# Kernel tuning notes

Hardware: AMD Instinct MI355X
Metric: run time of the kernel (lower is better)

The kernel has to match this reference:

```python
import jax, jax.numpy as jnp
import numpy as np

N_NODES = 100000
N_EDGES = 1600000
D_IN, D_H, D_OUT = 128, 64, 32


def _linear_init(key, out_dim, in_dim):
    # torch.nn.Linear default init: U(-1/sqrt(in), 1/sqrt(in))
    bound = 1.0 / np.sqrt(in_dim)
    return jax.random.uniform(key, (out_dim, in_dim), jnp.float32, -bound, bound)


def setup_inputs() -> dict:
    key = jax.random.key(0)
    ks = jax.random.split(key, 8)
    x = jax.random.normal(ks[0], (N_NODES, D_IN), dtype=jnp.float32)
    edge_index = jax.random.randint(ks[1], (2, N_EDGES), 0, N_NODES, dtype=jnp.int64)
    return {
        "x": x,
        "edge_index": edge_index,
        # SAGEConv layer 1: lin_l (neighbor agg, with bias), lin_r (root, no bias)
        "W1_l": _linear_init(ks[2], D_H, D_IN),
        "b1": jnp.zeros((D_H,), jnp.float32),
        "W1_r": _linear_init(ks[3], D_H, D_IN),
        # SAGEConv layer 2
        "W2_l": _linear_init(ks[4], D_OUT, D_H),
        "b2": jnp.zeros((D_OUT,), jnp.float32),
        "W2_r": _linear_init(ks[5], D_OUT, D_H),
    }


def _sage_conv(x, src, dst, W_l, b_l, W_r):
    """PyG SAGEConv with mean aggregation: lin_l(mean_{j in N(i)} x_j) + lin_r(x_i)."""
    n = x.shape[0]
    # scatter-mean of source features onto destination nodes
    agg = jax.ops.segment_sum(x[src], dst, num_segments=n)          # [N, d]
    deg = jax.ops.segment_sum(jnp.ones_like(dst, dtype=x.dtype), dst, num_segments=n)
    mean = agg / jnp.maximum(deg, 1.0)[:, None]
    return mean @ W_l.T + b_l + x @ W_r.T


def reference(x, edge_index, W1_l, b1, W1_r, W2_l, b2, W2_r):
    src, dst = edge_index[0], edge_index[1]
    h = _sage_conv(x, src, dst, W1_l, b1, W1_r)
    h = jax.nn.relu(h)
    # dropout p=0.5 is identity in eval mode
    return _sage_conv(h, src, dst, W2_l, b2, W2_r)
```

## Files before the change

kernel.cpp:

```cpp
#include <hip/hip_runtime.h>


namespace {
constexpr int N = 100000;
constexpr int E = 1600000;
constexpr int NBLK = (N + 255) / 256;
constexpr int NT16 = N / 16;
constexpr int NCHUNK = 64;
constexpr int CHUNK_N = 1600;
constexpr int CAP = 28000;
constexpr int PA_BLOCKS = 256;
constexpr int PER_BLK = E / PA_BLOCKS;
}

using bf16x8 = __attribute__((ext_vector_type(8))) short;
using f32x4  = __attribute__((ext_vector_type(4))) float;

__device__ __forceinline__ unsigned short f2bf(float f) {
    unsigned u = __builtin_bit_cast(unsigned, f);
    u += 0x7FFFu + ((u >> 16) & 1u);
    return (unsigned short)(u >> 16);
}

__device__ __forceinline__ bf16x8 load_frag8(const float* __restrict__ p) {
    const float4* p4 = (const float4*)p;
    float4 f0 = p4[0], f1 = p4[1];
    bf16x8 r;
    r[0] = f2bf(f0.x); r[1] = f2bf(f0.y); r[2] = f2bf(f0.z); r[3] = f2bf(f0.w);
    r[4] = f2bf(f1.x); r[5] = f2bf(f1.y); r[6] = f2bf(f1.z); r[7] = f2bf(f1.w);
    return r;
}

__device__ __forceinline__ float pk_lo(unsigned u) {
    return __builtin_bit_cast(float, u << 16);
}
__device__ __forceinline__ float pk_hi(unsigned u) {
    return __builtin_bit_cast(float, u & 0xFFFF0000u);
}
__device__ __forceinline__ unsigned pk2(float a, float b) {
    return (unsigned)f2bf(a) | ((unsigned)f2bf(b) << 16);
}


__global__ __launch_bounds__(256) void detect_dtype(const int* __restrict__ raw,
                                                    int* __restrict__ flag,
                                                    int* __restrict__ bcur) {
    if (threadIdx.x < NCHUNK) bcur[threadIdx.x] = 0;
    int any = 0;
#pragma unroll
    for (int k = 0; k < 64; ++k) {
        int i = threadIdx.x + k * 256;
        any |= raw[2 * i + 1];
    }
    unsigned long long b = __ballot(any != 0);
    __shared__ int acc[4];
    int w = threadIdx.x >> 6;
    if ((threadIdx.x & 63) == 0) acc[w] = (b != 0ULL) ? 1 : 0;
    __syncthreads();
    if (threadIdx.x == 0) *flag = acc[0] | acc[1] | acc[2] | acc[3];
}

__global__ __launch_bounds__(256) void bucket_edges(
        const int* __restrict__ raw, const int* __restrict__ flag,
        int* __restrict__ bcur, int2* __restrict__ bucket) {
    __shared__ int cnt[NCHUNK];
    __shared__ int res[NCHUNK];
    if (threadIdx.x < NCHUNK) cnt[threadIdx.x] = 0;
    __syncthreads();
    const int is32 = *flag;
    const int e0 = blockIdx.x * PER_BLK;
    for (int i = threadIdx.x; i < PER_BLK; i += 256) {
        int e = e0 + i;
        int d = is32 ? raw[E + e] : raw[2 * ((long long)E + e)];
        atomicAdd(&cnt[d / CHUNK_N], 1);
    }
    __syncthreads();
    if (threadIdx.x < NCHUNK) {
        res[threadIdx.x] = atomicAdd(&bcur[threadIdx.x], cnt[threadIdx.x]);
        cnt[threadIdx.x] = 0;
    }
    __syncthreads();
    for (int i = threadIdx.x; i < PER_BLK; i += 256) {
        int e = e0 + i;
        int d, s;
        if (is32) { d = raw[E + e]; s = raw[e]; }
        else      { d = raw[2 * ((long long)E + e)]; s = raw[2 * (long long)e]; }
        int c = d / CHUNK_N;
        int pos = res[c] + atomicAdd(&cnt[c], 1);
        if (pos < CAP) bucket[(size_t)c * CAP + pos] = make_int2(s, d);
    }
}

__global__ __launch_bounds__(1024) void count2(
        const int* __restrict__ bcur, const int2* __restrict__ bucket,
        int* __restrict__ counts) {
    __shared__ int scnt[CHUNK_N];
    const int chunk = blockIdx.x;
    const int lo = chunk * CHUNK_N;
    for (int i = threadIdx.x; i < CHUNK_N; i += 1024) scnt[i] = 0;
    __syncthreads();
    int n = bcur[chunk]; if (n > CAP) n = CAP;
    const int2* b = bucket + (size_t)chunk * CAP;
    for (int i = threadIdx.x; i < n; i += 1024)
        atomicAdd(&scnt[b[i].y - lo], 1);
    __syncthreads();
    const int lim = N - lo;
    for (int i = threadIdx.x; i < CHUNK_N; i += 1024)
        if (i < lim) counts[lo + i] = scnt[i];
}

__global__ __launch_bounds__(256) void scan1(const int* __restrict__ counts,
                                             int* __restrict__ rowstart,
                                             int* __restrict__ bsum) {
    __shared__ int tmp[256];
    int t = threadIdx.x;
    int i = blockIdx.x * 256 + t;
    int v = (i < N) ? counts[i] : 0;
    tmp[t] = v;
    __syncthreads();
#pragma unroll
    for (int off = 1; off < 256; off <<= 1) {
        int a = (t >= off) ? tmp[t - off] : 0;
        __syncthreads();
        tmp[t] += a;
        __syncthreads();
    }
    if (i < N) rowstart[i] = tmp[t] - v;
    if (t == 255) bsum[blockIdx.x] = tmp[255];
}

__global__ __launch_bounds__(512) void scan2(int* __restrict__ bsum) {
    __shared__ int tmp[512];
    int t = threadIdx.x;
    int v = (t < NBLK) ? bsum[t] : 0;
    tmp[t] = v;
    __syncthreads();
#pragma unroll
    for (int off = 1; off < 512; off <<= 1) {
        int a = (t >= off) ? tmp[t - off] : 0;
        __syncthreads();
        tmp[t] += a;
        __syncthreads();
    }
    if (t < NBLK) bsum[t] = tmp[t] - v;
}

__global__ void scan3(int* __restrict__ rowstart, const int* __restrict__ bsum) {
    int i = blockIdx.x * blockDim.x + threadIdx.x;
    if (i < N) rowstart[i] += bsum[i >> 8];
    if (i == 0) rowstart[N] = E;
}

__global__ __launch_bounds__(1024) void fill2(
        const int* __restrict__ bcur, const int2* __restrict__ bucket,
        const int* __restrict__ rowstart, int* __restrict__ csr) {
    __shared__ int scur[CHUNK_N];
    const int chunk = blockIdx.x;
    const int lo = chunk * CHUNK_N;
    const int lim = N - lo;
    for (int i = threadIdx.x; i < CHUNK_N; i += 1024)
        scur[i] = (i < lim) ? rowstart[lo + i] : 0;
    __syncthreads();
    int n = bcur[chunk]; if (n > CAP) n = CAP;
    const int2* b = bucket + (size_t)chunk * CAP;
    for (int i = threadIdx.x; i < n; i += 1024) {
        int2 sd = b[i];
        int pos = atomicAdd(&scur[sd.y - lo], 1);
        csr[pos] = sd.x;
    }
}

__global__ __launch_bounds__(256) void transform1_mfma(
        const float* __restrict__ x, const float* __restrict__ W1l,
        const float* __restrict__ W1r, unsigned short* __restrict__ z1b,
        float* __restrict__ r1) {
    const int lane = threadIdx.x & 63;
    const int gw = blockIdx.x * 4 + (threadIdx.x >> 6);
    const int q = gw & 1;
    const int r16 = lane & 15;
    const int kgrp = lane >> 4;

    bf16x8 wf[2][2][4];
#pragma unroll
    for (int m = 0; m < 2; ++m) {
        const float* W = m ? W1r : W1l;
#pragma unroll
        for (int c = 0; c < 2; ++c) {
            const float* pw = W + (size_t)(q * 32 + c * 16 + r16) * 128 + kgrp * 8;
#pragma unroll
            for (int kb = 0; kb < 4; ++kb)
                wf[m][c][kb] = load_frag8(pw + kb * 32);
        }
    }

    const int stride = (gridDim.x * 4) >> 1;
    for (int t = gw >> 1; t < NT16; t += stride) {
        const float* px = x + ((size_t)t * 16 + r16) * 128 + kgrp * 8;
        bf16x8 af[4];
#pragma unroll
        for (int kb = 0; kb < 4; ++kb) af[kb] = load_frag8(px + kb * 32);

        f32x4 a00 = {0.f,0.f,0.f,0.f}, a01 = {0.f,0.f,0.f,0.f};
        f32x4 a10 = {0.f,0.f,0.f,0.f}, a11 = {0.f,0.f,0.f,0.f};
#pragma unroll
        for (int kb = 0; kb < 4; ++kb) {
            a00 = __builtin_amdgcn_mfma_f32_16x16x32_bf16(af[kb], wf[0][0][kb], a00, 0, 0, 0);
            a01 = __builtin_amdgcn_mfma_f32_16x16x32_bf16(af[kb], wf[0][1][kb], a01, 0, 0, 0);
            a10 = __builtin_amdgcn_mfma_f32_16x16x32_bf16(af[kb], wf[1][0][kb], a10, 0, 0, 0);
            a11 = __builtin_amdgcn_mfma_f32_16x16x32_bf16(af[kb], wf[1][1][kb], a11, 0, 0, 0);
        }
#pragma unroll
        for (int i = 0; i < 4; ++i) {
            size_t row = (size_t)t * 16 + kgrp * 4 + i;
            z1b[row * 64 + q * 32 +  0 + r16] = f2bf(a00[i]);
            z1b[row * 64 + q * 32 + 16 + r16] = f2bf(a01[i]);
            r1[row * 64 + q * 32 +  0 + r16] = a10[i];
            r1[row * 64 + q * 32 + 16 + r16] = a11[i];
        }
    }
}

__global__ __launch_bounds__(256) void transform2_mfma(
        const unsigned short* __restrict__ hb, const float* __restrict__ W2l,
        const float* __restrict__ W2r, unsigned short* __restrict__ z2b,
        float* __restrict__ r2) {
    const int lane = threadIdx.x & 63;
    const int gw = blockIdx.x * 4 + (threadIdx.x >> 6);
    const int r16 = lane & 15;
    const int kgrp = lane >> 4;

    bf16x8 wf[2][2][2];
#pragma unroll
    for (int m = 0; m < 2; ++m) {
        const float* W = m ? W2r : W2l;
#pragma unroll
        for (int c = 0; c < 2; ++c) {
            const float* pw = W + (size_t)(c * 16 + r16) * 64 + kgrp * 8;
#pragma unroll
            for (int kb = 0; kb < 2; ++kb)
                wf[m][c][kb] = load_frag8(pw + kb * 32);
        }
    }

    for (int t = gw; t < NT16; t += gridDim.x * 4) {
        const unsigned short* ph = hb + ((size_t)t * 16 + r16) * 64 + kgrp * 8;
        bf16x8 af[2];
        af[0] = *(const bf16x8*)(ph);
        af[1] = *(const bf16x8*)(ph + 32);

        f32x4 a00 = {0.f,0.f,0.f,0.f}, a01 = {0.f,0.f,0.f,0.f};
        f32x4 a10 = {0.f,0.f,0.f,0.f}, a11 = {0.f,0.f,0.f,0.f};
#pragma unroll
        for (int kb = 0; kb < 2; ++kb) {
            a00 = __builtin_amdgcn_mfma_f32_16x16x32_bf16(af[kb], wf[0][0][kb], a00, 0, 0, 0);
            a01 = __builtin_amdgcn_mfma_f32_16x16x32_bf16(af[kb], wf[0][1][kb], a01, 0, 0, 0);
            a10 = __builtin_amdgcn_mfma_f32_16x16x32_bf16(af[kb], wf[1][0][kb], a10, 0, 0, 0);
            a11 = __builtin_amdgcn_mfma_f32_16x16x32_bf16(af[kb], wf[1][1][kb], a11, 0, 0, 0);
        }
#pragma unroll
        for (int i = 0; i < 4; ++i) {
            size_t row = (size_t)t * 16 + kgrp * 4 + i;
            z2b[row * 32 +  0 + r16] = f2bf(a00[i]);
            z2b[row * 32 + 16 + r16] = f2bf(a01[i]);
            r2[row * 32 +  0 + r16] = a10[i];
            r2[row * 32 + 16 + r16] = a11[i];
        }
    }
}

__global__ __launch_bounds__(256) void agg1_fused(
        const int* __restrict__ rowstart, const int* __restrict__ csr,
        const uint2* __restrict__ z1d, const float* __restrict__ r1,
        const float* __restrict__ b1, uint2* __restrict__ hb) {
    const int n = blockIdx.x * 4 + (threadIdx.x >> 6);
    if (n >= N) return;
    const int lane = threadIdx.x & 63;
    const int quad = lane >> 4;
    const int fl = lane & 15;
    const int beg = rowstart[n], end = rowstart[n + 1];
    float a0 = 0.f, a1 = 0.f, a2 = 0.f, a3 = 0.f;
    int p = beg;
    for (; p + 8 <= end; p += 8) {
        int c0 = csr[p + quad], c1 = csr[p + 4 + quad];
        uint2 u0 = z1d[(size_t)c0 * 16 + fl];
        uint2 u1 = z1d[(size_t)c1 * 16 + fl];
        a0 += pk_lo(u0.x) + pk_lo(u1.x);
        a1 += pk_hi(u0.x) + pk_hi(u1.x);
        a2 += pk_lo(u0.y) + pk_lo(u1.y);
        a3 += pk_hi(u0.y) + pk_hi(u1.y);
    }
    for (; p + 4 <= end; p += 4) {
        int c = csr[p + quad];
        uint2 u = z1d[(size_t)c * 16 + fl];
        a0 += pk_lo(u.x); a1 += pk_hi(u.x);
        a2 += pk_lo(u.y); a3 += pk_hi(u.y);
    }
    if (p < end) {
        int rem = end - p;
        if (quad < rem) {
            int c = csr[p + quad];
            uint2 u = z1d[(size_t)c * 16 + fl];
            a0 += pk_lo(u.x); a1 += pk_hi(u.x);
            a2 += pk_lo(u.y); a3 += pk_hi(u.y);
        }
    }
    a0 += __shfl_xor(a0, 16, 64); a1 += __shfl_xor(a1, 16, 64);
    a2 += __shfl_xor(a2, 16, 64); a3 += __shfl_xor(a3, 16, 64);
    a0 += __shfl_xor(a0, 32, 64); a1 += __shfl_xor(a1, 32, 64);
    a2 += __shfl_xor(a2, 32, 64); a3 += __shfl_xor(a3, 32, 64);
    if (lane < 16) {
        float inv = (end > beg) ? 1.0f / (float)(end - beg) : 0.f;
        float4 rv = ((const float4*)r1)[(size_t)n * 16 + fl];
        float4 bv = ((const float4*)b1)[fl];
        float h0 = fmaxf(a0 * inv + bv.x + rv.x, 0.f);
        float h1 = fmaxf(a1 * inv + bv.y + rv.y, 0.f);
        float h2 = fmaxf(a2 * inv + bv.z + rv.z, 0.f);
        float h3 = fmaxf(a3 * inv + bv.w + rv.w, 0.f);
        uint2 o;
        o.x = pk2(h0, h1);
        o.y = pk2(h2, h3);
        hb[(size_t)n * 16 + fl] = o;
    }
}

__global__ __launch_bounds__(256) void agg2_fused(
        const int* __restrict__ rowstart, const int* __restrict__ csr,
        const uint2* __restrict__ z2d, const float* __restrict__ r2,
        const float* __restrict__ b2, float* __restrict__ out) {
    const int n = blockIdx.x * 4 + (threadIdx.x >> 6);
    if (n >= N) return;
    const int lane = threadIdx.x & 63;
    const int oct = lane >> 3;
    const int fl = lane & 7;
    const int beg = rowstart[n], end = rowstart[n + 1];
    float a0 = 0.f, a1 = 0.f, a2 = 0.f, a3 = 0.f;
    int p = beg;
    for (; p + 8 <= end; p += 8) {
        int c = csr[p + oct];
        uint2 u = z2d[(size_t)c * 8 + fl];
        a0 += pk_lo(u.x); a1 += pk_hi(u.x);
        a2 += pk_lo(u.y); a3 += pk_hi(u.y);
    }
    if (p < end) {
        int rem = end - p;
        if (oct < rem) {
            int c = csr[p + oct];
            uint2 u = z2d[(size_t)c * 8 + fl];
            a0 += pk_lo(u.x); a1 += pk_hi(u.x);
            a2 += pk_lo(u.y); a3 += pk_hi(u.y);
        }
    }
    a0 += __shfl_xor(a0, 8, 64);  a1 += __shfl_xor(a1, 8, 64);
    a2 += __shfl_xor(a2, 8, 64);  a3 += __shfl_xor(a3, 8, 64);
    a0 += __shfl_xor(a0, 16, 64); a1 += __shfl_xor(a1, 16, 64);
    a2 += __shfl_xor(a2, 16, 64); a3 += __shfl_xor(a3, 16, 64);
    a0 += __shfl_xor(a0, 32, 64); a1 += __shfl_xor(a1, 32, 64);
    a2 += __shfl_xor(a2, 32, 64); a3 += __shfl_xor(a3, 32, 64);
    if (lane < 8) {
        float inv = (end > beg) ? 1.0f / (float)(end - beg) : 0.f;
        float4 rv = ((const float4*)r2)[(size_t)n * 8 + fl];
        float4 bv = ((const float4*)b2)[fl];
        float4 o;
        o.x = a0 * inv + bv.x + rv.x;
        o.y = a1 * inv + bv.y + rv.y;
        o.z = a2 * inv + bv.z + rv.z;
        o.w = a3 * inv + bv.w + rv.w;
        ((float4*)out)[(size_t)n * 8 + fl] = o;
    }
}


extern "C" void kernel_launch(void* const* d_in, const int* in_sizes, int n_in,
                              void* d_out, int out_size, void* d_ws, size_t ws_size,
                              hipStream_t stream) {
    const float* x    = (const float*)d_in[0];
    const int*   raw  = (const int*)d_in[1];
    const float* W1l  = (const float*)d_in[2];
    const float* b1   = (const float*)d_in[3];
    const float* W1r  = (const float*)d_in[4];
    const float* W2l  = (const float*)d_in[5];
    const float* b2   = (const float*)d_in[6];
    const float* W2r  = (const float*)d_in[7];
    float* out = (float*)d_out;

    char* wsb = (char*)d_ws;
    unsigned short* z1b = (unsigned short*)wsb;
    unsigned short* z2b = (unsigned short*)wsb;
    float* r1 = (float*)(wsb + 16 * 1024 * 1024);
    float* r2 = (float*)(wsb + 16 * 1024 * 1024);
    unsigned short* hb = (unsigned short*)(wsb + 48 * 1024 * 1024);
    int2* bucket = (int2*)(wsb + 64 * 1024 * 1024);

    int* ibase    = (int*)(wsb + 80 * 1024 * 1024);
    int* counts   = ibase;
    int* rowstart = ibase + N;
    int* bsum     = ibase + 2 * N + 1;
    int* csr      = ibase + 2 * N + 1 + 512;
    int* flag     = csr + E;
    int* bcur     = flag + 1;

    detect_dtype<<<1, 256, 0, stream>>>(raw, flag, bcur);
    bucket_edges<<<PA_BLOCKS, 256, 0, stream>>>(raw, flag, bcur, bucket);
    count2<<<NCHUNK, 1024, 0, stream>>>(bcur, bucket, counts);
    scan1<<<NBLK, 256, 0, stream>>>(counts, rowstart, bsum);
    scan2<<<1, 512, 0, stream>>>(bsum);
    scan3<<<NBLK, 256, 0, stream>>>(rowstart, bsum);
    fill2<<<NCHUNK, 1024, 0, stream>>>(bcur, bucket, rowstart, csr);

    transform1_mfma<<<1024, 256, 0, stream>>>(x, W1l, W1r, z1b, r1);
    agg1_fused<<<(N + 3) / 4, 256, 0, stream>>>(rowstart, csr, (const uint2*)z1b, r1, b1, (uint2*)hb);

    transform2_mfma<<<1024, 256, 0, stream>>>(hb, W2l, W2r, z2b, r2);
    agg2_fused<<<(N + 3) / 4, 256, 0, stream>>>(rowstart, csr, (const uint2*)z2b, r2, b2, out);
}
```

Baseline: 206.5 us.

## Fuse CSR count/scan/fill into one kernel, store root terms as bf16, unroll gather

Replaces the five CSR-construction kernels (count, three-stage scan, fill) with one per-chunk kernel. Each chunk gets its global base by summing earlier bucket counts, then does its own shared-memory scan, which removes launches and the global counts/bsum round trips. The root-term outputs r1/r2 are now stored as bf16 instead of fp32, halving that traffic at some precision cost. The layer-1 gather loop is unrolled to 16 edges per iteration for more memory-level parallelism.

```diff
diff --git a/kernel.cpp b/kernel.cpp
--- a/kernel.cpp
+++ b/kernel.cpp
@@ -4,7 +4,6 @@
 namespace {
 constexpr int N = 100000;
 constexpr int E = 1600000;
-constexpr int NBLK = (N + 255) / 256;
 constexpr int NT16 = N / 16;
 constexpr int NCHUNK = 64;
 constexpr int CHUNK_N = 1600;
@@ -91,81 +90,48 @@
     }
 }
 
-__global__ __launch_bounds__(1024) void count2(
+__global__ __launch_bounds__(1024) void build_csr(
         const int* __restrict__ bcur, const int2* __restrict__ bucket,
-        int* __restrict__ counts) {
-    __shared__ int scnt[CHUNK_N];
+        int* __restrict__ rowstart, int* __restrict__ csr) {
+    __shared__ int sc[2048];
+    __shared__ int st[2048];
+    __shared__ int sbase;
     const int chunk = blockIdx.x;
     const int lo = chunk * CHUNK_N;
-    for (int i = threadIdx.x; i < CHUNK_N; i += 1024) scnt[i] = 0;
+    const int t = threadIdx.x;
+    sc[t] = 0; sc[t + 1024] = 0;
+    if (t == 0) {
+        int bsum = 0;
+        for (int c = 0; c < chunk; ++c) bsum += bcur[c];
+        sbase = bsum;
+    }
     __syncthreads();
     int n = bcur[chunk]; if (n > CAP) n = CAP;
     const int2* b = bucket + (size_t)chunk * CAP;
-    for (int i = threadIdx.x; i < n; i += 1024)
-        atomicAdd(&scnt[b[i].y - lo], 1);
-    __syncthreads();
+    for (int i = t; i < n; i += 1024)
+        atomicAdd(&sc[b[i].y - lo], 1);
+    __syncthreads();
+    const int cA = sc[t], cB = sc[t + 1024];
+    int* src = sc; int* dst = st;
+    for (int off = 1; off < 2048; off <<= 1) {
+        int vA = src[t] + ((t >= off) ? src[t - off] : 0);
+        int vB = src[t + 1024] + src[t + 1024 - off];
+        dst[t] = vA; dst[t + 1024] = vB;
+        __syncthreads();
+        int* tmp = src; src = dst; dst = tmp;
+    }
+    const int base = sbase;
+    const int exA = base + src[t] - cA;
+    const int exB = base + src[t + 1024] - cB;
     const int lim = N - lo;
-    for (int i = threadIdx.x; i < CHUNK_N; i += 1024)
-        if (i < lim) counts[lo + i] = scnt[i];
-}
-
-__global__ __launch_bounds__(256) void scan1(const int* __restrict__ counts,
-                                             int* __restrict__ rowstart,
-                                             int* __restrict__ bsum) {
-    __shared__ int tmp[256];
-    int t = threadIdx.x;
-    int i = blockIdx.x * 256 + t;
-    int v = (i < N) ? counts[i] : 0;
-    tmp[t] = v;
-    __syncthreads();
-#pragma unroll
-    for (int off = 1; off < 256; off <<= 1) {
-        int a = (t >= off) ? tmp[t - off] : 0;
-        __syncthreads();
-        tmp[t] += a;
-        __syncthreads();
-    }
-    if (i < N) rowstart[i] = tmp[t] - v;
-    if (t == 255) bsum[blockIdx.x] = tmp[255];
-}
-
-__global__ __launch_bounds__(512) void scan2(int* __restrict__ bsum) {
-    __shared__ int tmp[512];
-    int t = threadIdx.x;
-    int v = (t < NBLK) ? bsum[t] : 0;
-    tmp[t] = v;
-    __syncthreads();
-#pragma unroll
-    for (int off = 1; off < 512; off <<= 1) {
-        int a = (t >= off) ? tmp[t - off] : 0;
-        __syncthreads();
-        tmp[t] += a;
-        __syncthreads();
-    }
-    if (t < NBLK) bsum[t] = tmp[t] - v;
-}
-
-__global__ void scan3(int* __restrict__ rowstart, const int* __restrict__ bsum) {
-    int i = blockIdx.x * blockDim.x + threadIdx.x;
-    if (i < N) rowstart[i] += bsum[i >> 8];
-    if (i == 0) rowstart[N] = E;
-}
-
-__global__ __launch_bounds__(1024) void fill2(
-        const int* __restrict__ bcur, const int2* __restrict__ bucket,
-        const int* __restrict__ rowstart, int* __restrict__ csr) {
-    __shared__ int scur[CHUNK_N];
-    const int chunk = blockIdx.x;
-    const int lo = chunk * CHUNK_N;
-    const int lim = N - lo;
-    for (int i = threadIdx.x; i < CHUNK_N; i += 1024)
-        scur[i] = (i < lim) ? rowstart[lo + i] : 0;
-    __syncthreads();
-    int n = bcur[chunk]; if (n > CAP) n = CAP;
-    const int2* b = bucket + (size_t)chunk * CAP;
-    for (int i = threadIdx.x; i < n; i += 1024) {
+    if (t < lim) rowstart[lo + t] = exA;
+    if (t + 1024 < CHUNK_N && t + 1024 < lim) rowstart[lo + t + 1024] = exB;
+    if (chunk == 0 && t == 0) rowstart[N] = E;
+    dst[t] = exA; dst[t + 1024] = exB;
+    __syncthreads();
+    for (int i = t; i < n; i += 1024) {
         int2 sd = b[i];
-        int pos = atomicAdd(&scur[sd.y - lo], 1);
+        int pos = atomicAdd(&dst[sd.y - lo], 1);
         csr[pos] = sd.x;
     }
 }
@@ -173,7 +139,7 @@
 __global__ __launch_bounds__(256) void transform1_mfma(
         const float* __restrict__ x, const float* __restrict__ W1l,
         const float* __restrict__ W1r, unsigned short* __restrict__ z1b,
-        float* __restrict__ r1) {
+        unsigned short* __restrict__ r1b) {
     const int lane = threadIdx.x & 63;
     const int gw = blockIdx.x * 4 + (threadIdx.x >> 6);
     const int q = gw & 1;
@@ -214,8 +180,8 @@
             size_t row = (size_t)t * 16 + kgrp * 4 + i;
             z1b[row * 64 + q * 32 +  0 + r16] = f2bf(a00[i]);
             z1b[row * 64 + q * 32 + 16 + r16] = f2bf(a01[i]);
-            r1[row * 64 + q * 32 +  0 + r16] = a10[i];
-            r1[row * 64 + q * 32 + 16 + r16] = a11[i];
+            r1b[row * 64 + q * 32 +  0 + r16] = f2bf(a10[i]);
+            r1b[row * 64 + q * 32 + 16 + r16] = f2bf(a11[i]);
         }
     }
 }
@@ -223,7 +189,7 @@
 __global__ __launch_bounds__(256) void transform2_mfma(
         const unsigned short* __restrict__ hb, const float* __restrict__ W2l,
         const float* __restrict__ W2r, unsigned short* __restrict__ z2b,
-        float* __restrict__ r2) {
+        unsigned short* __restrict__ r2b) {
     const int lane = threadIdx.x & 63;
     const int gw = blockIdx.x * 4 + (threadIdx.x >> 6);
     const int r16 = lane & 15;
@@ -262,15 +228,15 @@
             size_t row = (size_t)t * 16 + kgrp * 4 + i;
             z2b[row * 32 +  0 + r16] = f2bf(a00[i]);
             z2b[row * 32 + 16 + r16] = f2bf(a01[i]);
-            r2[row * 32 +  0 + r16] = a10[i];
-            r2[row * 32 + 16 + r16] = a11[i];
+            r2b[row * 32 +  0 + r16] = f2bf(a10[i]);
+            r2b[row * 32 + 16 + r16] = f2bf(a11[i]);
         }
     }
 }
 
 __global__ __launch_bounds__(256) void agg1_fused(
         const int* __restrict__ rowstart, const int* __restrict__ csr,
-        const uint2* __restrict__ z1d, const float* __restrict__ r1,
+        const uint2* __restrict__ z1d, const uint2* __restrict__ r1d,
         const float* __restrict__ b1, uint2* __restrict__ hb) {
     const int n = blockIdx.x * 4 + (threadIdx.x >> 6);
     if (n >= N) return;
@@ -280,14 +246,17 @@
     const int beg = rowstart[n], end = rowstart[n + 1];
     float a0 = 0.f, a1 = 0.f, a2 = 0.f, a3 = 0.f;
     int p = beg;
-    for (; p + 8 <= end; p += 8) {
-        int c0 = csr[p + quad], c1 = csr[p + 4 + quad];
+    for (; p + 16 <= end; p += 16) {
+        int c0 = csr[p + quad],      c1 = csr[p + 4 + quad];
+        int c2 = csr[p + 8 + quad],  c3 = csr[p + 12 + quad];
         uint2 u0 = z1d[(size_t)c0 * 16 + fl];
         uint2 u1 = z1d[(size_t)c1 * 16 + fl];
-        a0 += pk_lo(u0.x) + pk_lo(u1.x);
-        a1 += pk_hi(u0.x) + pk_hi(u1.x);
-        a2 += pk_lo(u0.y) + pk_lo(u1.y);
-        a3 += pk_hi(u0.y) + pk_hi(u1.y);
+        uint2 u2 = z1d[(size_t)c2 * 16 + fl];
+        uint2 u3 = z1d[(size_t)c3 * 16 + fl];
+        a0 += pk_lo(u0.x) + pk_lo(u1.x) + pk_lo(u2.x) + pk_lo(u3.x);
+        a1 += pk_hi(u0.x) + pk_hi(u1.x) + pk_hi(u2.x) + pk_hi(u3.x);
+        a2 += pk_lo(u0.y) + pk_lo(u1.y) + pk_lo(u2.y) + pk_lo(u3.y);
+        a3 += pk_hi(u0.y) + pk_hi(u1.y) + pk_hi(u2.y) + pk_hi(u3.y);
     }
     for (; p + 4 <= end; p += 4) {
         int c = csr[p + quad];
@@ -310,12 +279,12 @@
     a2 += __shfl_xor(a2, 32, 64); a3 += __shfl_xor(a3, 32, 64);
     if (lane < 16) {
         float inv = (end > beg) ? 1.0f / (float)(end - beg) : 0.f;
-        float4 rv = ((const float4*)r1)[(size_t)n * 16 + fl];
+        uint2 rr = r1d[(size_t)n * 16 + fl];
         float4 bv = ((const float4*)b1)[fl];
-        float h0 = fmaxf(a0 * inv + bv.x + rv.x, 0.f);
-        float h1 = fmaxf(a1 * inv + bv.y + rv.y, 0.f);
-        float h2 = fmaxf(a2 * inv + bv.z + rv.z, 0.f);
-        float h3 = fmaxf(a3 * inv + bv.w + rv.w, 0.f);
+        float h0 = fmaxf(a0 * inv + bv.x + pk_lo(rr.x), 0.f);
+        float h1 = fmaxf(a1 * inv + bv.y + pk_hi(rr.x), 0.f);
+        float h2 = fmaxf(a2 * inv + bv.z + pk_lo(rr.y), 0.f);
+        float h3 = fmaxf(a3 * inv + bv.w + pk_hi(rr.y), 0.f);
         uint2 o;
         o.x = pk2(h0, h1);
         o.y = pk2(h2, h3);
@@ -325,7 +294,7 @@
 
 __global__ __launch_bounds__(256) void agg2_fused(
         const int* __restrict__ rowstart, const int* __restrict__ csr,
-        const uint2* __restrict__ z2d, const float* __restrict__ r2,
+        const uint2* __restrict__ z2d, const uint2* __restrict__ r2d,
         const float* __restrict__ b2, float* __restrict__ out) {
     const int n = blockIdx.x * 4 + (threadIdx.x >> 6);
     if (n >= N) return;
@@ -358,13 +327,13 @@
     a2 += __shfl_xor(a2, 32, 64); a3 += __shfl_xor(a3, 32, 64);
     if (lane < 8) {
         float inv = (end > beg) ? 1.0f / (float)(end - beg) : 0.f;
-        float4 rv = ((const float4*)r2)[(size_t)n * 8 + fl];
+        uint2 rr = r2d[(size_t)n * 8 + fl];
         float4 bv = ((const float4*)b2)[fl];
         float4 o;
-        o.x = a0 * inv + bv.x + rv.x;
-        o.y = a1 * inv + bv.y + rv.y;
-        o.z = a2 * inv + bv.z + rv.z;
-        o.w = a3 * inv + bv.w + rv.w;
+        o.x = a0 * inv + bv.x + pk_lo(rr.x);
+        o.y = a1 * inv + bv.y + pk_hi(rr.x);
+        o.z = a2 * inv + bv.z + pk_lo(rr.y);
+        o.w = a3 * inv + bv.w + pk_hi(rr.y);
         ((float4*)out)[(size_t)n * 8 + fl] = o;
     }
 }
@@ -386,30 +355,26 @@
     char* wsb = (char*)d_ws;
     unsigned short* z1b = (unsigned short*)wsb;
     unsigned short* z2b = (unsigned short*)wsb;
-    float* r1 = (float*)(wsb + 16 * 1024 * 1024);
-    float* r2 = (float*)(wsb + 16 * 1024 * 1024);
-    unsigned short* hb = (unsigned short*)(wsb + 48 * 1024 * 1024);
+    unsigned short* r1b = (unsigned short*)(wsb + 16 * 1024 * 1024);
+    unsigned short* r2b = (unsigned short*)(wsb + 16 * 1024 * 1024);
+    unsigned short* hb  = (unsigned short*)(wsb + 48 * 1024 * 1024);
     int2* bucket = (int2*)(wsb + 64 * 1024 * 1024);
 
     int* ibase    = (int*)(wsb + 80 * 1024 * 1024);
-    int* counts   = ibase;
-    int* rowstart = ibase + N;
-    int* bsum     = ibase + 2 * N + 1;
-    int* csr      = ibase + 2 * N + 1 + 512;
+    int* rowstart = ibase;
+    int* csr      = ibase + N + 1;
     int* flag     = csr + E;
     int* bcur     = flag + 1;
 
     detect_dtype<<<1, 256, 0, stream>>>(raw, flag, bcur);
     bucket_edges<<<PA_BLOCKS, 256, 0, stream>>>(raw, flag, bcur, bucket);
-    count2<<<NCHUNK, 1024, 0, stream>>>(bcur, bucket, counts);
-    scan1<<<NBLK, 256, 0, stream>>>(counts, rowstart, bsum);
-    scan2<<<1, 512, 0, stream>>>(bsum);
-    scan3<<<NBLK, 256, 0, stream>>>(rowstart, bsum);
-    fill2<<<NCHUNK, 1024, 0, stream>>>(bcur, bucket, rowstart, csr);
-
-    transform1_mfma<<<1024, 256, 0, stream>>>(x, W1l, W1r, z1b, r1);
-    agg1_fused<<<(N + 3) / 4, 256, 0, stream>>>(rowstart, csr, (const uint2*)z1b, r1, b1, (uint2*)hb);
-
-    transform2_mfma<<<1024, 256, 0, stream>>>(hb, W2l, W2r, z2b, r2);
-    agg2_fused<<<(N + 3) / 4, 256, 0, stream>>>(rowstart, csr, (const uint2*)z2b, r2, b2, out);
-}
+    build_csr<<<NCHUNK, 1024, 0, stream>>>(bcur, bucket, rowstart, csr);
+
+    transform1_mfma<<<1024, 256, 0, stream>>>(x, W1l, W1r, z1b, r1b);
+    agg1_fused<<<(N + 3) / 4, 256, 0, stream>>>(rowstart, csr, (const uint2*)z1b,
+                                                (const uint2*)r1b, b1, (uint2*)hb);
+
+    transform2_mfma<<<1024, 256, 0, stream>>>(hb, W2l, W2r, z2b, r2b);
+    agg2_fused<<<(N + 3) / 4, 256, 0, stream>>>(rowstart, csr, (const uint2*)z2b,
+                                                (const uint2*)r2b, b2, out);
+}
```

Result: faster. 200.3 us (-3.0%).
